# Kernel tuning notes

Measured on AMD Instinct MI355X. Metric: run time of the kernel, lower is better.

## Reference

```python
import jax, jax.numpy as jnp
import numpy as np

B, S, E, H = 4, 2048, 512, 8
DK = E // H
LN_EPS = 1e-5


def setup_inputs() -> dict:
    key = jax.random.key(0)
    ks = jax.random.split(key, 12)
    s_in = 1.0 / np.sqrt(E)
    inp = {
        "Q": jax.random.normal(ks[0], (B, S, E), jnp.float32),
        "K": jax.random.normal(ks[1], (B, S, E), jnp.float32),
        "V": jax.random.normal(ks[2], (B, S, E), jnp.float32),
        # per-head projection weights stacked over heads: [H, E, DK]
        "Wq": jax.random.normal(ks[3], (H, E, DK), jnp.float32) * s_in,
        "bq": jnp.zeros((H, DK), jnp.float32),
        "Wk": jax.random.normal(ks[4], (H, E, DK), jnp.float32) * s_in,
        "bk": jnp.zeros((H, DK), jnp.float32),
        "Wv": jax.random.normal(ks[5], (H, E, DK), jnp.float32) * s_in,
        "bv": jnp.zeros((H, DK), jnp.float32),
        # final linear: [E, E]
        "Wf": jax.random.normal(ks[6], (E, E), jnp.float32) * s_in,
        "bf": jnp.zeros((E,), jnp.float32),
        "gamma": jnp.ones((E,), jnp.float32),
        "beta": jnp.zeros((E,), jnp.float32),
    }
    return inp


def reference(Q, K, V, Wq, bq, Wk, bk, Wv, bv, Wf, bf, gamma, beta):
    scale = DK ** (-0.5)
    # batched per-head projections: [B,H,S,DK]
    q = jnp.einsum("bse,hed->bhsd", Q, Wq) + bq[None, :, None, :]
    k = jnp.einsum("bse,hed->bhsd", K, Wk) + bk[None, :, None, :]
    v = jnp.einsum("bse,hed->bhsd", V, Wv) + bv[None, :, None, :]
    # full QK^T scores [B,H,S,S], scaled, softmax over key axis (dim=2 of bmm == last)
    scores = jnp.einsum("bhsd,bhtd->bhst", q, k) * scale
    attn = jax.nn.softmax(scores, axis=-1)
    ctx = jnp.einsum("bhst,bhtd->bhsd", attn, v)
    # concat heads along feature dim -> [B,S,E]
    z = jnp.transpose(ctx, (0, 2, 1, 3)).reshape(B, S, E)
    residual = jnp.einsum("bse,ef->bsf", z, Wf) + bf
    x = Q + residual
    mean = jnp.mean(x, axis=-1, keepdims=True)
    var = jnp.mean(jnp.square(x - mean), axis=-1, keepdims=True)
    out = (x - mean) * jax.lax.rsqrt(var + LN_EPS) * gamma + beta
    return out
```

## Files before the change

### kernel.cpp

```cpp
#include <hip/hip_runtime.h>
#include <hip/hip_bf16.h>

#define Bb 4
#define Ss 2048
#define Ee 512
#define Hh 8
#define DKk 64

typedef __bf16 bf16_t;
typedef bf16_t bf16x8 __attribute__((ext_vector_type(8)));
typedef bf16_t bf16x4 __attribute__((ext_vector_type(4)));
typedef float f32x4 __attribute__((ext_vector_type(4)));
typedef float f32x16 __attribute__((ext_vector_type(16)));

#define MFMA16(a, b, c) __builtin_amdgcn_mfma_f32_16x16x32_bf16(a, b, c, 0, 0, 0)
#define MFMA32(a, b, c) __builtin_amdgcn_mfma_f32_32x32x16_bf16(a, b, c, 0, 0, 0)

#define GLOAD16(src, dst)                                          \
  __builtin_amdgcn_global_load_lds(                                \
      (const __attribute__((address_space(1))) void*)(src),        \
      (__attribute__((address_space(3))) void*)(dst), 16, 0, 0)

#define LO4(v) __builtin_shufflevector(v, v, 0, 1, 2, 3)
#define HI4(v) __builtin_shufflevector(v, v, 4, 5, 6, 7)

static __device__ __forceinline__ bf16_t f2bf(float f) { return (bf16_t)f; }

static __device__ __forceinline__ float fast_exp2(float x) {
#if __has_builtin(__builtin_amdgcn_exp2f)
  return __builtin_amdgcn_exp2f(x);
#else
  return exp2f(x);
#endif
}

static __device__ __forceinline__ unsigned cvtpk(float lo, float hi) {
  unsigned r;
  asm("v_cvt_pk_bf16_f32 %0, %1, %2" : "=v"(r) : "v"(lo), "v"(hi));
  return r;
}
static __device__ __forceinline__ void plswap(unsigned& a, unsigned& b) {
  asm("v_permlane32_swap_b32 %0, %1" : "+v"(a), "+v"(b));
}

__global__ __launch_bounds__(256) void cvt_k(const float* __restrict__ Q,
                                             const float* __restrict__ K,
                                             const float* __restrict__ V,
                                             bf16_t* __restrict__ dst) {
  int which = blockIdx.x >> 11;
  int bi = blockIdx.x & 2047;
  const float* src = (which == 0) ? Q : ((which == 1) ? K : V);
  bf16_t* d = dst + (size_t)which * ((size_t)Bb * Ss * Ee);
  size_t idx = ((size_t)bi * 256 + threadIdx.x) * 8;
  float4 a = *(const float4*)(src + idx);
  float4 b = *(const float4*)(src + idx + 4);
  bf16x8 o;
  o[0] = f2bf(a.x); o[1] = f2bf(a.y); o[2] = f2bf(a.z); o[3] = f2bf(a.w);
  o[4] = f2bf(b.x); o[5] = f2bf(b.y); o[6] = f2bf(b.z); o[7] = f2bf(b.w);
  *(bf16x8*)(d + idx) = o;
}

__global__ __launch_bounds__(256) void pack_weights_k(
    const float* __restrict__ Wq, const float* __restrict__ Wk,
    const float* __restrict__ Wv, const float* __restrict__ Wf,
    bf16_t* __restrict__ Wt, bf16_t* __restrict__ Wft) {
  __shared__ float tile[64][65];
  int t = threadIdx.x;
  int y = blockIdx.y;
  const float* sp;
  bf16_t* dp;
  int sR, r0, c0;
  if (y < 24) {
    int mat = y >> 3, h = y & 7;
    const float* W = (mat == 0) ? Wq : ((mat == 1) ? Wk : Wv);
    sp = W + (size_t)h * (Ee * DKk);
    sR = 64;
    dp = Wt + (size_t)mat * (Ee * Ee) + (size_t)(h * 64) * Ee;
    r0 = blockIdx.x * 64;
    c0 = 0;
  } else {
    sp = Wf;
    sR = 512;
    dp = Wft;
    r0 = blockIdx.x * 64;
    c0 = (y - 24) * 64;
  }
  int lr = t >> 2, seg = t & 3;
  const float* sprow = sp + (size_t)(r0 + lr) * sR + c0 + seg * 16;
  float4 f0 = ((const float4*)sprow)[0];
  float4 f1 = ((const float4*)sprow)[1];
  float4 f2 = ((const float4*)sprow)[2];
  float4 f3 = ((const float4*)sprow)[3];
  tile[lr][seg * 16 + 0] = f0.x;  tile[lr][seg * 16 + 1] = f0.y;
  tile[lr][seg * 16 + 2] = f0.z;  tile[lr][seg * 16 + 3] = f0.w;
  tile[lr][seg * 16 + 4] = f1.x;  tile[lr][seg * 16 + 5] = f1.y;
  tile[lr][seg * 16 + 6] = f1.z;  tile[lr][seg * 16 + 7] = f1.w;
  tile[lr][seg * 16 + 8] = f2.x;  tile[lr][seg * 16 + 9] = f2.y;
  tile[lr][seg * 16 + 10] = f2.z; tile[lr][seg * 16 + 11] = f2.w;
  tile[lr][seg * 16 + 12] = f3.x; tile[lr][seg * 16 + 13] = f3.y;
  tile[lr][seg * 16 + 14] = f3.z; tile[lr][seg * 16 + 15] = f3.w;
  __syncthreads();
  bf16x8 o0, o1;
#pragma unroll
  for (int i = 0; i < 8; i++) {
    o0[i] = f2bf(tile[seg * 16 + i][lr]);
    o1[i] = f2bf(tile[seg * 16 + 8 + i][lr]);
  }
  bf16_t* dst = dp + (size_t)(c0 + lr) * Ee + r0 + seg * 16;
  *(bf16x8*)dst = o0;
  *(bf16x8*)(dst + 8) = o1;
}

__global__ __launch_bounds__(256) void vt_k(const bf16_t* __restrict__ vsrc,
                                            bf16_t* __restrict__ vtG) {
  __shared__ bf16_t tile[64][68];
  const int t = threadIdx.x;
  const int bh = blockIdx.y;
  const int s0 = blockIdx.x * 64;
  const bf16_t* vp = vsrc + (size_t)bh * (Ss * DKk);
  const int r = t >> 2, seg = t & 3;
  const bf16_t* src = vp + (size_t)(s0 + r) * DKk + seg * 16;
  bf16x8 a = ((const bf16x8*)src)[0];
  bf16x8 b = ((const bf16x8*)src)[1];
  bf16_t* ld = &tile[r][seg * 16];
  *(bf16x4*)(ld + 0) = LO4(a); *(bf16x4*)(ld + 4) = HI4(a);
  *(bf16x4*)(ld + 8) = LO4(b); *(bf16x4*)(ld + 12) = HI4(b);
  __syncthreads();
  bf16x8 o0, o1;
#pragma unroll
  for (int j = 0; j < 8; j++) {
    o0[j] = tile[seg * 16 + j][r];
    o1[j] = tile[seg * 16 + 8 + j][r];
  }
  bf16_t* dst = vtG + (size_t)bh * ((size_t)DKk * Ss) + (size_t)r * Ss + s0 + seg * 16;
  *(bf16x8*)dst = o0;
  *(bf16x8*)(dst + 8) = o1;
}

__global__ __launch_bounds__(256) void proj_gemm_k(
    const bf16_t* __restrict__ Xb3, const bf16_t* __restrict__ Wt,
    const float* __restrict__ bq, const float* __restrict__ bk,
    const float* __restrict__ bv, bf16_t* __restrict__ qkv) {
  __shared__ bf16_t As[128 * 64];
  __shared__ bf16_t Bs[128 * 64];
  const int t = threadIdx.x;
  const int zb = blockIdx.z;
  const bf16_t* Ap = Wt + (size_t)zb * (Ee * Ee);
  const bf16_t* Bp = Xb3 + (size_t)zb * ((size_t)Bb * Ss * Ee);
  const float* bias = (zb == 0) ? bq : ((zb == 1) ? bk : bv);
  bf16_t* Outp = qkv + (size_t)zb * ((size_t)Bb * Hh * Ss * DKk);
  const float scl = (zb == 0) ? 0.18033688f : 1.0f;
  const int id = blockIdx.x + (blockIdx.y << 2);
  const int nid = (id & 7) * 32 + (id >> 3);
  const int n0 = (nid & 3) * 128;
  const int m0 = (nid >> 2) * 128;
  const int lane = t & 63, w = t >> 6;
  const int wn = w >> 1, wm = w & 1;
  const int rsel = lane & 15, grp = lane >> 4;
  const int wbase = (t & ~63);

  f32x4 acc[4][4];
#pragma unroll
  for (int ni = 0; ni < 4; ni++)
#pragma unroll
    for (int mi = 0; mi < 4; mi++) acc[ni][mi] = (f32x4){0.f, 0.f, 0.f, 0.f};

  for (int k0 = 0; k0 < Ee; k0 += 64) {
#pragma unroll
    for (int i = 0; i < 4; i++) {
      int slot = i * 256 + t;
      int row = slot >> 3;
      int g = (slot & 7) ^ (row & 7);
      GLOAD16(Ap + (size_t)(n0 + row) * Ee + k0 + g * 8,
              As + (size_t)(i * 256 + wbase) * 8);
      GLOAD16(Bp + (size_t)(m0 + row) * Ee + k0 + g * 8,
              Bs + (size_t)(i * 256 + wbase) * 8);
    }
    __syncthreads();
#pragma unroll
    for (int kk = 0; kk < 2; kk++) {
      bf16x8 af[4], bff[4];
#pragma unroll
      for (int ni = 0; ni < 4; ni++) {
        int arow = wn * 64 + ni * 16 + rsel;
        int c = ((kk * 4 + grp) ^ (arow & 7)) * 8;
        af[ni] = *(const bf16x8*)&As[arow * 64 + c];
      }
#pragma unroll
      for (int mi = 0; mi < 4; mi++) {
        int brow = wm * 64 + mi * 16 + rsel;
        int c = ((kk * 4 + grp) ^ (brow & 7)) * 8;
        bff[mi] = *(const bf16x8*)&Bs[brow * 64 + c];
      }
#pragma unroll
      for (int ni = 0; ni < 4; ni++)
#pragma unroll
        for (int mi = 0; mi < 4; mi++)
          acc[ni][mi] = MFMA16(af[ni], bff[mi], acc[ni][mi]);
    }
    __syncthreads();
  }

#pragma unroll
  for (int ni = 0; ni < 4; ni++) {
    int nb = n0 + wn * 64 + ni * 16 + grp * 4;
    float4 b4 = *(const float4*)(bias + nb);
    const float* b4p = (const float*)&b4;
    int hh = nb >> 6, dd = nb & 63;
#pragma unroll
    for (int mi = 0; mi < 4; mi++) {
      int m = m0 + wm * 64 + mi * 16 + rsel;
      int bI = m >> 11, sI = m & 2047;
      bf16x4 o;
#pragma unroll
      for (int r = 0; r < 4; r++)
        o[r] = f2bf((acc[ni][mi][r] + b4p[r]) * scl);
      *(bf16x4*)(Outp + (((size_t)(bI * Hh + hh)) * Ss + sI) * DKk + dd) = o;
    }
  }
}

__global__ __launch_bounds__(256) void final_gemm_k(
    const bf16_t* __restrict__ zin, const bf16_t* __restrict__ Wft,
    const float* __restrict__ bfb, const float* __restrict__ Qres,
    float* __restrict__ x) {
  __shared__ bf16_t As[128 * 64];
  __shared__ bf16_t Bs[128 * 64];
  const int t = threadIdx.x;
  const int id = blockIdx.x + (blockIdx.y << 2);
  const int nid = (id & 7) * 32 + (id >> 3);
  const int n0 = (nid & 3) * 128;
  const int m0 = (nid >> 2) * 128;
  const int lane = t & 63, w = t >> 6;
  const int wn = w >> 1, wm = w & 1;
  const int rsel = lane & 15, grp = lane >> 4;
  const int wbase = (t & ~63);

  f32x4 acc[4][4];
#pragma unroll
  for (int ni = 0; ni < 4; ni++)
#pragma unroll
    for (int mi = 0; mi < 4; mi++) acc[ni][mi] = (f32x4){0.f, 0.f, 0.f, 0.f};

  for (int k0 = 0; k0 < Ee; k0 += 64) {
#pragma unroll
    for (int i = 0; i < 4; i++) {
      int slot = i * 256 + t;
      int row = slot >> 3;
      int g = (slot & 7) ^ (row & 7);
      GLOAD16(Wft + (size_t)(n0 + row) * Ee + k0 + g * 8,
              As + (size_t)(i * 256 + wbase) * 8);
      GLOAD16(zin + (size_t)(m0 + row) * Ee + k0 + g * 8,
              Bs + (size_t)(i * 256 + wbase) * 8);
    }
    __syncthreads();
#pragma unroll
    for (int kk = 0; kk < 2; kk++) {
      bf16x8 af[4], bff[4];
#pragma unroll
      for (int ni = 0; ni < 4; ni++) {
        int arow = wn * 64 + ni * 16 + rsel;
        int c = ((kk * 4 + grp) ^ (arow & 7)) * 8;
        af[ni] = *(const bf16x8*)&As[arow * 64 + c];
      }
#pragma unroll
      for (int mi = 0; mi < 4; mi++) {
        int brow = wm * 64 + mi * 16 + rsel;
        int c = ((kk * 4 + grp) ^ (brow & 7)) * 8;
        bff[mi] = *(const bf16x8*)&Bs[brow * 64 + c];
      }
#pragma unroll
      for (int ni = 0; ni < 4; ni++)
#pragma unroll
        for (int mi = 0; mi < 4; mi++)
          acc[ni][mi] = MFMA16(af[ni], bff[mi], acc[ni][mi]);
    }
    __syncthreads();
  }

#pragma unroll
  for (int ni = 0; ni < 4; ni++) {
    int nb = n0 + wn * 64 + ni * 16 + grp * 4;
    float4 b4 = *(const float4*)(bfb + nb);
#pragma unroll
    for (int mi = 0; mi < 4; mi++) {
      int m = m0 + wm * 64 + mi * 16 + rsel;
      float4 q4 = *(const float4*)(Qres + (size_t)m * Ee + nb);
      float4 o;
      o.x = acc[ni][mi][0] + b4.x + q4.x;
      o.y = acc[ni][mi][1] + b4.y + q4.y;
      o.z = acc[ni][mi][2] + b4.z + q4.z;
      o.w = acc[ni][mi][3] + b4.w + q4.w;
      *(float4*)(x + (size_t)m * Ee + nb) = o;
    }
  }
}

__global__ __launch_bounds__(512, 4) void attn_k(const bf16_t* __restrict__ qkv,
                                                 const bf16_t* __restrict__ vtG,
                                                 bf16_t* __restrict__ zout) {
  const size_t HS = (size_t)Bb * Hh * Ss * DKk;
  __shared__ __align__(16) unsigned char smem_raw[2 * 34816];
  bf16_t (*Ks)[2][64][68] = reinterpret_cast<bf16_t (*)[2][64][68]>(smem_raw);
  bf16_t (*Vt)[2][64][68] = reinterpret_cast<bf16_t (*)[2][64][68]>(smem_raw + 34816);
  const int t = threadIdx.x, w = t >> 6, lane = t & 63;
  const int qsub = w >> 1, half = w & 1;
  const int ql = lane & 31, hi = lane >> 5;
  const int bh = blockIdx.y;
  const bf16_t* qp = qkv + (size_t)bh * (Ss * DKk);
  const bf16_t* kp = qp + HS;
  const bf16_t* vt = vtG + (size_t)bh * ((size_t)DKk * Ss);
  const int qrow = blockIdx.x * 128 + qsub * 32 + ql;

  bf16x8 qf0 = *(const bf16x8*)(qp + (size_t)qrow * DKk + 0 + hi * 8);
  bf16x8 qf1 = *(const bf16x8*)(qp + (size_t)qrow * DKk + 16 + hi * 8);
  bf16x8 qf2 = *(const bf16x8*)(qp + (size_t)qrow * DKk + 32 + hi * 8);
  bf16x8 qf3 = *(const bf16x8*)(qp + (size_t)qrow * DKk + 48 + hi * 8);

  const int sid = qsub * 64 + lane;
  const int srow = sid >> 2, sseg = sid & 3;
  const int koff0 = half * (Ss / 2);

  f32x16 ctx0, ctx1;
#pragma unroll
  for (int r = 0; r < 16; r++) { ctx0[r] = 0.f; ctx1[r] = 0.f; }
  float m_run = -1e30f, l_run = 0.f;

  {
    const bf16_t* ksrc = kp + (size_t)(koff0 + srow) * DKk + sseg * 16;
    bf16x8 ka = ((const bf16x8*)ksrc)[0], kb = ((const bf16x8*)ksrc)[1];
    const bf16_t* vsrc = vt + (size_t)srow * Ss + koff0 + sseg * 16;
    bf16x8 va = ((const bf16x8*)vsrc)[0], vb = ((const bf16x8*)vsrc)[1];
    bf16_t* kd = &Ks[half][0][srow][sseg * 16];
    *(bf16x4*)(kd + 0) = LO4(ka); *(bf16x4*)(kd + 4) = HI4(ka);
    *(bf16x4*)(kd + 8) = LO4(kb); *(bf16x4*)(kd + 12) = HI4(kb);
    bf16_t* vd = &Vt[half][0][srow][sseg * 16];
    *(bf16x4*)(vd + 0) = LO4(va); *(bf16x4*)(vd + 4) = HI4(va);
    *(bf16x4*)(vd + 8) = LO4(vb); *(bf16x4*)(vd + 12) = HI4(vb);
  }
  __syncthreads();

  const int NT = (Ss / 2) / 64;
  bf16x8 pk0, pk1, pv0, pv1;
  for (int it = 0; it < NT; ++it) {
    const int cb = it & 1;
    if (it < NT - 1) {
      const int k0 = koff0 + (it + 1) * 64;
      const bf16_t* ksrc = kp + (size_t)(k0 + srow) * DKk + sseg * 16;
      pk0 = ((const bf16x8*)ksrc)[0]; pk1 = ((const bf16x8*)ksrc)[1];
      const bf16_t* vsrc = vt + (size_t)srow * Ss + k0 + sseg * 16;
      pv0 = ((const bf16x8*)vsrc)[0]; pv1 = ((const bf16x8*)vsrc)[1];
    }

    f32x16 st0, st1;
#pragma unroll
    for (int r = 0; r < 16; r++) { st0[r] = 0.f; st1[r] = 0.f; }
    __builtin_amdgcn_s_setprio(1);
#pragma unroll
    for (int s = 0; s < 4; s++) {
      bf16x4 a0 = *(const bf16x4*)&Ks[half][cb][ql][s * 16 + hi * 8];
      bf16x4 a1 = *(const bf16x4*)&Ks[half][cb][ql][s * 16 + hi * 8 + 4];
      bf16x8 af = __builtin_shufflevector(a0, a1, 0, 1, 2, 3, 4, 5, 6, 7);
      bf16x4 c0 = *(const bf16x4*)&Ks[half][cb][32 + ql][s * 16 + hi * 8];
      bf16x4 c1 = *(const bf16x4*)&Ks[half][cb][32 + ql][s * 16 + hi * 8 + 4];
      bf16x8 af2 = __builtin_shufflevector(c0, c1, 0, 1, 2, 3, 4, 5, 6, 7);
      bf16x8 qf = (s == 0) ? qf0 : ((s == 1) ? qf1 : ((s == 2) ? qf2 : qf3));
      st0 = MFMA32(af, qf, st0);
      st1 = MFMA32(af2, qf, st1);
    }
    __builtin_amdgcn_s_setprio(0);

    float mx = st0[0];
#pragma unroll
    for (int r = 1; r < 16; r++) mx = fmaxf(mx, st0[r]);
#pragma unroll
    for (int r = 0; r < 16; r++) mx = fmaxf(mx, st1[r]);
    mx = fmaxf(mx, __shfl_xor(mx, 32));
    if (__any(mx > m_run + 8.0f)) {
      float mn = fmaxf(m_run, mx);
      float sc = fast_exp2(m_run - mn);
      l_run *= sc;
#pragma unroll
      for (int r = 0; r < 16; r++) { ctx0[r] *= sc; ctx1[r] *= sc; }
      m_run = mn;
    }
    float ps = 0.f;
#pragma unroll
    for (int r = 0; r < 16; r++) { st0[r] = fast_exp2(st0[r] - m_run); ps += st0[r]; }
#pragma unroll
    for (int r = 0; r < 16; r++) { st1[r] = fast_exp2(st1[r] - m_run); ps += st1[r]; }
    ps += __shfl_xor(ps, 32);
    l_run += ps;

    union U { unsigned u[4]; bf16x8 v; };
    U F00, F01, F10, F11;
    {
      unsigned x0 = cvtpk(st0[0], st0[1]), y0 = cvtpk(st0[4], st0[5]); plswap(x0, y0);
      unsigned x1 = cvtpk(st0[2], st0[3]), y1 = cvtpk(st0[6], st0[7]); plswap(x1, y1);
      F00.u[0] = x0; F00.u[1] = x1; F00.u[2] = y0; F00.u[3] = y1;
      unsigned x2 = cvtpk(st0[8], st0[9]), y2 = cvtpk(st0[12], st0[13]); plswap(x2, y2);
      unsigned x3 = cvtpk(st0[10], st0[11]), y3 = cvtpk(st0[14], st0[15]); plswap(x3, y3);
      F01.u[0] = x2; F01.u[1] = x3; F01.u[2] = y2; F01.u[3] = y3;
      unsigned x4 = cvtpk(st1[0], st1[1]), y4 = cvtpk(st1[4], st1[5]); plswap(x4, y4);
      unsigned x5 = cvtpk(st1[2], st1[3]), y5 = cvtpk(st1[6], st1[7]); plswap(x5, y5);
      F10.u[0] = x4; F10.u[1] = x5; F10.u[2] = y4; F10.u[3] = y5;
      unsigned x6 = cvtpk(st1[8], st1[9]), y6 = cvtpk(st1[12], st1[13]); plswap(x6, y6);
      unsigned x7 = cvtpk(st1[10], st1[11]), y7 = cvtpk(st1[14], st1[15]); plswap(x7, y7);
      F11.u[0] = x6; F11.u[1] = x7; F11.u[2] = y6; F11.u[3] = y7;
    }

    auto rdv = [&](int mtrow, int col) -> bf16x8 {
      bf16x4 lo4 = *(const bf16x4*)&Vt[half][cb][mtrow + ql][col + hi * 8];
      bf16x4 hi4 = *(const bf16x4*)&Vt[half][cb][mtrow + ql][col + hi * 8 + 4];
      return __builtin_shufflevector(lo4, hi4, 0, 1, 2, 3, 4, 5, 6, 7);
    };
    __builtin_amdgcn_s_setprio(1);
    ctx0 = MFMA32(rdv(0, 0), F00.v, ctx0);
    ctx0 = MFMA32(rdv(0, 16), F01.v, ctx0);
    ctx0 = MFMA32(rdv(0, 32), F10.v, ctx0);
    ctx0 = MFMA32(rdv(0, 48), F11.v, ctx0);
    ctx1 = MFMA32(rdv(32, 0), F00.v, ctx1);
    ctx1 = MFMA32(rdv(32, 16), F01.v, ctx1);
    ctx1 = MFMA32(rdv(32, 32), F10.v, ctx1);
    ctx1 = MFMA32(rdv(32, 48), F11.v, ctx1);
    __builtin_amdgcn_s_setprio(0);

    if (it < NT - 1) {
      bf16_t* kd = &Ks[half][cb ^ 1][srow][sseg * 16];
      *(bf16x4*)(kd + 0) = LO4(pk0); *(bf16x4*)(kd + 4) = HI4(pk0);
      *(bf16x4*)(kd + 8) = LO4(pk1); *(bf16x4*)(kd + 12) = HI4(pk1);
      bf16_t* vd = &Vt[half][cb ^ 1][srow][sseg * 16];
      *(bf16x4*)(vd + 0) = LO4(pv0); *(bf16x4*)(vd + 4) = HI4(pv0);
      *(bf16x4*)(vd + 8) = LO4(pv1); *(bf16x4*)(vd + 12) = HI4(pv1);
    }
    __syncthreads();
  }

  float* mr = (float*)smem_raw;
  const int msl = qsub * 64 + lane;
  float* cslot = mr + msl * 33;
  float* mym = mr + 8448;
  float* myl = mr + 8704;
  if (half == 1) {
#pragma unroll
    for (int r = 0; r < 16; r++) { cslot[r] = ctx0[r]; cslot[16 + r] = ctx1[r]; }
    mym[msl] = m_run;
    myl[msl] = l_run;
  }
  __syncthreads();
  if (half == 0) {
    float m1 = mym[msl], l1 = myl[msl];
    float mt = fmaxf(m_run, m1);
    float f0 = fast_exp2(m_run - mt), f1 = fast_exp2(m1 - mt);
    float inv = 1.f / (l_run * f0 + l1 * f1);
    const int bI = bh >> 3, hh = bh & 7;
    bf16_t* zr = zout + ((size_t)bI * Ss + qrow) * Ee + hh * 64;
#pragma unroll
    for (int a = 0; a < 4; a++) {
      bf16x4 o0, o1;
#pragma unroll
      for (int b2 = 0; b2 < 4; b2++) {
        o0[b2] = f2bf((ctx0[a * 4 + b2] * f0 + cslot[a * 4 + b2] * f1) * inv);
        o1[b2] = f2bf((ctx1[a * 4 + b2] * f0 + cslot[16 + a * 4 + b2] * f1) * inv);
      }
      *(bf16x4*)(zr + a * 8 + hi * 4) = o0;
      *(bf16x4*)(zr + 32 + a * 8 + hi * 4) = o1;
    }
  }
}

__global__ __launch_bounds__(256) void ln_k(
    const float* __restrict__ x, const float* __restrict__ gamma,
    const float* __restrict__ beta, float* __restrict__ out) {
  int row = blockIdx.x * 4 + (threadIdx.x >> 6);
  int lane = threadIdx.x & 63;
  const float* xr = x + (size_t)row * Ee;
  float4 v0 = *(const float4*)(xr + lane * 8);
  float4 v1 = *(const float4*)(xr + lane * 8 + 4);
  float s = v0.x + v0.y + v0.z + v0.w + v1.x + v1.y + v1.z + v1.w;
  float ss = v0.x * v0.x + v0.y * v0.y + v0.z * v0.z + v0.w * v0.w +
             v1.x * v1.x + v1.y * v1.y + v1.z * v1.z + v1.w * v1.w;
#pragma unroll
  for (int off = 32; off >= 1; off >>= 1) {
    s += __shfl_xor(s, off);
    ss += __shfl_xor(ss, off);
  }
  float mean = s * (1.f / 512.f);
  float var = ss * (1.f / 512.f) - mean * mean;
  float inv = rsqrtf(var + 1e-5f);
  float4 g0 = *(const float4*)(gamma + lane * 8);
  float4 g1 = *(const float4*)(gamma + lane * 8 + 4);
  float4 b0 = *(const float4*)(beta + lane * 8);
  float4 b1 = *(const float4*)(beta + lane * 8 + 4);
  float4 o0, o1;
  o0.x = (v0.x - mean) * inv * g0.x + b0.x;
  o0.y = (v0.y - mean) * inv * g0.y + b0.y;
  o0.z = (v0.z - mean) * inv * g0.z + b0.z;
  o0.w = (v0.w - mean) * inv * g0.w + b0.w;
  o1.x = (v1.x - mean) * inv * g1.x + b1.x;
  o1.y = (v1.y - mean) * inv * g1.y + b1.y;
  o1.z = (v1.z - mean) * inv * g1.z + b1.z;
  o1.w = (v1.w - mean) * inv * g1.w + b1.w;
  float* orow = out + (size_t)row * Ee;
  *(float4*)(orow + lane * 8) = o0;
  *(float4*)(orow + lane * 8 + 4) = o1;
}

extern "C" void kernel_launch(void* const* d_in, const int* in_sizes, int n_in,
                              void* d_out, int out_size, void* d_ws, size_t ws_size,
                              hipStream_t stream) {
  const float* Q = (const float*)d_in[0];
  const float* K = (const float*)d_in[1];
  const float* V = (const float*)d_in[2];
  const float* Wq = (const float*)d_in[3];
  const float* bq = (const float*)d_in[4];
  const float* Wk = (const float*)d_in[5];
  const float* bk = (const float*)d_in[6];
  const float* Wv = (const float*)d_in[7];
  const float* bv = (const float*)d_in[8];
  const float* Wf = (const float*)d_in[9];
  const float* bfb = (const float*)d_in[10];
  const float* gamma = (const float*)d_in[11];
  const float* beta = (const float*)d_in[12];
  float* out = (float*)d_out;

  bf16_t* Wt = (bf16_t*)d_ws;
  bf16_t* Wft = Wt + 3 * Ee * Ee;
  bf16_t* qkv = Wft + Ee * Ee;
  bf16_t* sA = qkv + (size_t)3 * Bb * Hh * Ss * DKk;
  bf16_t* z = sA;
  bf16_t* vtG = sA + (size_t)Bb * Hh * Ss * DKk;
  float* x = (float*)qkv;

  cvt_k<<<dim3(6144), dim3(256), 0, stream>>>(Q, K, V, sA);
  pack_weights_k<<<dim3(8, 32), dim3(256), 0, stream>>>(Wq, Wk, Wv, Wf, Wt, Wft);
  proj_gemm_k<<<dim3(4, 64, 3), dim3(256), 0, stream>>>(sA, Wt, bq, bk, bv, qkv);
  vt_k<<<dim3(32, 32), dim3(256), 0, stream>>>(qkv + (size_t)2 * Bb * Hh * Ss * DKk, vtG);
  attn_k<<<dim3(16, 32), dim3(512), 0, stream>>>(qkv, vtG, z);
  final_gemm_k<<<dim3(4, 64), dim3(256), 0, stream>>>(z, Wft, bfb, Q, x);
  ln_k<<<dim3(2048), dim3(256), 0, stream>>>(x, gamma, beta, out);
}
```

Before: 208.0 us.

## Fuse input conversion and V transpose into projection GEMM, shrink GEMM tiles

Removes the separate fp32-to-bf16 conversion kernel by having the projection GEMM load fp32 Q/K/V and convert them in registers before writing to LDS. It also removes the V transpose kernel by writing V directly in transposed layout from the GEMM epilogue. GEMM tiles shrink from 128x128 to 64x64 to get more blocks. The intermediate before layer norm is stored as bf16 instead of fp32, and the softmax max/sum reductions are reassociated. The risks are scattered strided stores for V, lower data reuse per tile, and reduced precision in the residual before layer norm.

```diff
diff --git a/kernel.cpp b/kernel.cpp
--- a/kernel.cpp
+++ b/kernel.cpp
@@ -34,6 +34,10 @@
 #endif
 }
 
+static __device__ __forceinline__ float max3f(float a, float b, float c) {
+  return fmaxf(fmaxf(a, b), c);
+}
+
 static __device__ __forceinline__ unsigned cvtpk(float lo, float hi) {
   unsigned r;
   asm("v_cvt_pk_bf16_f32 %0, %1, %2" : "=v"(r) : "v"(lo), "v"(hi));
@@ -41,23 +45,6 @@
 }
 static __device__ __forceinline__ void plswap(unsigned& a, unsigned& b) {
   asm("v_permlane32_swap_b32 %0, %1" : "+v"(a), "+v"(b));
-}
-
-__global__ __launch_bounds__(256) void cvt_k(const float* __restrict__ Q,
-                                             const float* __restrict__ K,
-                                             const float* __restrict__ V,
-                                             bf16_t* __restrict__ dst) {
-  int which = blockIdx.x >> 11;
-  int bi = blockIdx.x & 2047;
-  const float* src = (which == 0) ? Q : ((which == 1) ? K : V);
-  bf16_t* d = dst + (size_t)which * ((size_t)Bb * Ss * Ee);
-  size_t idx = ((size_t)bi * 256 + threadIdx.x) * 8;
-  float4 a = *(const float4*)(src + idx);
-  float4 b = *(const float4*)(src + idx + 4);
-  bf16x8 o;
-  o[0] = f2bf(a.x); o[1] = f2bf(a.y); o[2] = f2bf(a.z); o[3] = f2bf(a.w);
-  o[4] = f2bf(b.x); o[5] = f2bf(b.y); o[6] = f2bf(b.z); o[7] = f2bf(b.w);
-  *(bf16x8*)(d + idx) = o;
 }
 
 __global__ __launch_bounds__(256) void pack_weights_k(
@@ -111,111 +98,117 @@
   *(bf16x8*)(dst + 8) = o1;
 }
 
-__global__ __launch_bounds__(256) void vt_k(const bf16_t* __restrict__ vsrc,
-                                            bf16_t* __restrict__ vtG) {
-  __shared__ bf16_t tile[64][68];
-  const int t = threadIdx.x;
-  const int bh = blockIdx.y;
-  const int s0 = blockIdx.x * 64;
-  const bf16_t* vp = vsrc + (size_t)bh * (Ss * DKk);
-  const int r = t >> 2, seg = t & 3;
-  const bf16_t* src = vp + (size_t)(s0 + r) * DKk + seg * 16;
-  bf16x8 a = ((const bf16x8*)src)[0];
-  bf16x8 b = ((const bf16x8*)src)[1];
-  bf16_t* ld = &tile[r][seg * 16];
-  *(bf16x4*)(ld + 0) = LO4(a); *(bf16x4*)(ld + 4) = HI4(a);
-  *(bf16x4*)(ld + 8) = LO4(b); *(bf16x4*)(ld + 12) = HI4(b);
-  __syncthreads();
-  bf16x8 o0, o1;
-#pragma unroll
-  for (int j = 0; j < 8; j++) {
-    o0[j] = tile[seg * 16 + j][r];
-    o1[j] = tile[seg * 16 + 8 + j][r];
-  }
-  bf16_t* dst = vtG + (size_t)bh * ((size_t)DKk * Ss) + (size_t)r * Ss + s0 + seg * 16;
-  *(bf16x8*)dst = o0;
-  *(bf16x8*)(dst + 8) = o1;
-}
-
 __global__ __launch_bounds__(256) void proj_gemm_k(
-    const bf16_t* __restrict__ Xb3, const bf16_t* __restrict__ Wt,
+    const float* __restrict__ Qi, const float* __restrict__ Ki,
+    const float* __restrict__ Vi, const bf16_t* __restrict__ Wt,
     const float* __restrict__ bq, const float* __restrict__ bk,
-    const float* __restrict__ bv, bf16_t* __restrict__ qkv) {
-  __shared__ bf16_t As[128 * 64];
-  __shared__ bf16_t Bs[128 * 64];
+    const float* __restrict__ bv, bf16_t* __restrict__ qk,
+    bf16_t* __restrict__ vtG) {
+  __shared__ bf16_t As[64 * 64];
+  __shared__ bf16_t Bs[64 * 64];
   const int t = threadIdx.x;
   const int zb = blockIdx.z;
   const bf16_t* Ap = Wt + (size_t)zb * (Ee * Ee);
-  const bf16_t* Bp = Xb3 + (size_t)zb * ((size_t)Bb * Ss * Ee);
+  const float* Bp = (zb == 0) ? Qi : ((zb == 1) ? Ki : Vi);
   const float* bias = (zb == 0) ? bq : ((zb == 1) ? bk : bv);
-  bf16_t* Outp = qkv + (size_t)zb * ((size_t)Bb * Hh * Ss * DKk);
   const float scl = (zb == 0) ? 0.18033688f : 1.0f;
-  const int id = blockIdx.x + (blockIdx.y << 2);
-  const int nid = (id & 7) * 32 + (id >> 3);
-  const int n0 = (nid & 3) * 128;
-  const int m0 = (nid >> 2) * 128;
+  const int id = blockIdx.x + (blockIdx.y << 3);
+  const int nid = (id & 7) * 128 + (id >> 3);
+  const int n0 = (nid & 7) * 64;
+  const int m0 = (nid >> 3) * 64;
   const int lane = t & 63, w = t >> 6;
   const int wn = w >> 1, wm = w & 1;
   const int rsel = lane & 15, grp = lane >> 4;
   const int wbase = (t & ~63);
 
-  f32x4 acc[4][4];
-#pragma unroll
-  for (int ni = 0; ni < 4; ni++)
-#pragma unroll
-    for (int mi = 0; mi < 4; mi++) acc[ni][mi] = (f32x4){0.f, 0.f, 0.f, 0.f};
-
+  f32x4 acc[2][2];
+#pragma unroll
+  for (int ni = 0; ni < 2; ni++)
+#pragma unroll
+    for (int mi = 0; mi < 2; mi++) acc[ni][mi] = (f32x4){0.f, 0.f, 0.f, 0.f};
+
+  const int row2 = t >> 3, j2 = t & 7;
   for (int k0 = 0; k0 < Ee; k0 += 64) {
 #pragma unroll
-    for (int i = 0; i < 4; i++) {
+    for (int i = 0; i < 2; i++) {
       int slot = i * 256 + t;
       int row = slot >> 3;
       int g = (slot & 7) ^ (row & 7);
       GLOAD16(Ap + (size_t)(n0 + row) * Ee + k0 + g * 8,
               As + (size_t)(i * 256 + wbase) * 8);
-      GLOAD16(Bp + (size_t)(m0 + row) * Ee + k0 + g * 8,
-              Bs + (size_t)(i * 256 + wbase) * 8);
+    }
+#pragma unroll
+    for (int i = 0; i < 2; i++) {
+      int row = row2 + i * 32;
+      int g = j2 ^ (row & 7);
+      const float* src = Bp + (size_t)(m0 + row) * Ee + k0 + g * 8;
+      float4 fa = ((const float4*)src)[0];
+      float4 fb = ((const float4*)src)[1];
+      union { unsigned u[4]; bf16x8 v; } P;
+      P.u[0] = cvtpk(fa.x, fa.y); P.u[1] = cvtpk(fa.z, fa.w);
+      P.u[2] = cvtpk(fb.x, fb.y); P.u[3] = cvtpk(fb.z, fb.w);
+      *(bf16x8*)&Bs[(row * 8 + j2) * 8] = P.v;
     }
     __syncthreads();
 #pragma unroll
     for (int kk = 0; kk < 2; kk++) {
-      bf16x8 af[4], bff[4];
-#pragma unroll
-      for (int ni = 0; ni < 4; ni++) {
-        int arow = wn * 64 + ni * 16 + rsel;
+      bf16x8 af[2], bff[2];
+#pragma unroll
+      for (int ni = 0; ni < 2; ni++) {
+        int arow = wn * 32 + ni * 16 + rsel;
         int c = ((kk * 4 + grp) ^ (arow & 7)) * 8;
         af[ni] = *(const bf16x8*)&As[arow * 64 + c];
       }
 #pragma unroll
-      for (int mi = 0; mi < 4; mi++) {
-        int brow = wm * 64 + mi * 16 + rsel;
+      for (int mi = 0; mi < 2; mi++) {
+        int brow = wm * 32 + mi * 16 + rsel;
         int c = ((kk * 4 + grp) ^ (brow & 7)) * 8;
         bff[mi] = *(const bf16x8*)&Bs[brow * 64 + c];
       }
 #pragma unroll
-      for (int ni = 0; ni < 4; ni++)
-#pragma unroll
-        for (int mi = 0; mi < 4; mi++)
+      for (int ni = 0; ni < 2; ni++)
+#pragma unroll
+        for (int mi = 0; mi < 2; mi++)
           acc[ni][mi] = MFMA16(af[ni], bff[mi], acc[ni][mi]);
     }
     __syncthreads();
   }
 
-#pragma unroll
-  for (int ni = 0; ni < 4; ni++) {
-    int nb = n0 + wn * 64 + ni * 16 + grp * 4;
-    float4 b4 = *(const float4*)(bias + nb);
-    const float* b4p = (const float*)&b4;
-    int hh = nb >> 6, dd = nb & 63;
-#pragma unroll
-    for (int mi = 0; mi < 4; mi++) {
-      int m = m0 + wm * 64 + mi * 16 + rsel;
-      int bI = m >> 11, sI = m & 2047;
-      bf16x4 o;
-#pragma unroll
-      for (int r = 0; r < 4; r++)
-        o[r] = f2bf((acc[ni][mi][r] + b4p[r]) * scl);
-      *(bf16x4*)(Outp + (((size_t)(bI * Hh + hh)) * Ss + sI) * DKk + dd) = o;
+  if (zb < 2) {
+    bf16_t* Outp = qk + (size_t)zb * ((size_t)Bb * Hh * Ss * DKk);
+#pragma unroll
+    for (int ni = 0; ni < 2; ni++) {
+      int nb = n0 + wn * 32 + ni * 16 + grp * 4;
+      float4 b4 = *(const float4*)(bias + nb);
+      const float* b4p = (const float*)&b4;
+      int hh = nb >> 6, dd = nb & 63;
+#pragma unroll
+      for (int mi = 0; mi < 2; mi++) {
+        int m = m0 + wm * 32 + mi * 16 + rsel;
+        int bI = m >> 11, sI = m & 2047;
+        bf16x4 o;
+#pragma unroll
+        for (int r = 0; r < 4; r++)
+          o[r] = f2bf((acc[ni][mi][r] + b4p[r]) * scl);
+        *(bf16x4*)(Outp + (((size_t)(bI * Hh + hh)) * Ss + sI) * DKk + dd) = o;
+      }
+    }
+  } else {
+#pragma unroll
+    for (int ni = 0; ni < 2; ni++) {
+      int nb = n0 + wn * 32 + ni * 16 + grp * 4;
+      float4 b4 = *(const float4*)(bias + nb);
+      const float* b4p = (const float*)&b4;
+      int hh = nb >> 6, dd = nb & 63;
+#pragma unroll
+      for (int mi = 0; mi < 2; mi++) {
+        int m = m0 + wm * 32 + mi * 16 + rsel;
+        int bI = m >> 11, sI = m & 2047;
+        bf16_t* base = vtG + (((size_t)(bI * Hh + hh)) * 64 + dd) * Ss + sI;
+#pragma unroll
+        for (int r = 0; r < 4; r++)
+          base[(size_t)r * Ss] = f2bf(acc[ni][mi][r] + b4p[r]);
+      }
     }
   }
 }
@@ -223,28 +216,28 @@
 __global__ __launch_bounds__(256) void final_gemm_k(
     const bf16_t* __restrict__ zin, const bf16_t* __restrict__ Wft,
     const float* __restrict__ bfb, const float* __restrict__ Qres,
-    float* __restrict__ x) {
-  __shared__ bf16_t As[128 * 64];
-  __shared__ bf16_t Bs[128 * 64];
+    bf16_t* __restrict__ x) {
+  __shared__ bf16_t As[64 * 64];
+  __shared__ bf16_t Bs[64 * 64];
   const int t = threadIdx.x;
-  const int id = blockIdx.x + (blockIdx.y << 2);
-  const int nid = (id & 7) * 32 + (id >> 3);
-  const int n0 = (nid & 3) * 128;
-  const int m0 = (nid >> 2) * 128;
+  const int id = blockIdx.x + (blockIdx.y << 3);
+  const int nid = (id & 7) * 128 + (id >> 3);
+  const int n0 = (nid & 7) * 64;
+  const int m0 = (nid >> 3) * 64;
   const int lane = t & 63, w = t >> 6;
   const int wn = w >> 1, wm = w & 1;
   const int rsel = lane & 15, grp = lane >> 4;
   const int wbase = (t & ~63);
 
-  f32x4 acc[4][4];
-#pragma unroll
-  for (int ni = 0; ni < 4; ni++)
-#pragma unroll
-    for (int mi = 0; mi < 4; mi++) acc[ni][mi] = (f32x4){0.f, 0.f, 0.f, 0.f};
+  f32x4 acc[2][2];
+#pragma unroll
+  for (int ni = 0; ni < 2; ni++)
+#pragma unroll
+    for (int mi = 0; mi < 2; mi++) acc[ni][mi] = (f32x4){0.f, 0.f, 0.f, 0.f};
 
   for (int k0 = 0; k0 < Ee; k0 += 64) {
 #pragma unroll
-    for (int i = 0; i < 4; i++) {
+    for (int i = 0; i < 2; i++) {
       int slot = i * 256 + t;
       int row = slot >> 3;
       int g = (slot & 7) ^ (row & 7);
@@ -256,47 +249,47 @@
     __syncthreads();
 #pragma unroll
     for (int kk = 0; kk < 2; kk++) {
-      bf16x8 af[4], bff[4];
-#pragma unroll
-      for (int ni = 0; ni < 4; ni++) {
-        int arow = wn * 64 + ni * 16 + rsel;
+      bf16x8 af[2], bff[2];
+#pragma unroll
+      for (int ni = 0; ni < 2; ni++) {
+        int arow = wn * 32 + ni * 16 + rsel;
         int c = ((kk * 4 + grp) ^ (arow & 7)) * 8;
         af[ni] = *(const bf16x8*)&As[arow * 64 + c];
       }
 #pragma unroll
-      for (int mi = 0; mi < 4; mi++) {
-        int brow = wm * 64 + mi * 16 + rsel;
+      for (int mi = 0; mi < 2; mi++) {
+        int brow = wm * 32 + mi * 16 + rsel;
         int c = ((kk * 4 + grp) ^ (brow & 7)) * 8;
         bff[mi] = *(const bf16x8*)&Bs[brow * 64 + c];
       }
 #pragma unroll
-      for (int ni = 0; ni < 4; ni++)
-#pragma unroll
-        for (int mi = 0; mi < 4; mi++)
+      for (int ni = 0; ni < 2; ni++)
+#pragma unroll
+        for (int mi = 0; mi < 2; mi++)
           acc[ni][mi] = MFMA16(af[ni], bff[mi], acc[ni][mi]);
     }
     __syncthreads();
   }
 
 #pragma unroll
-  for (int ni = 0; ni < 4; ni++) {
-    int nb = n0 + wn * 64 + ni * 16 + grp * 4;
+  for (int ni = 0; ni < 2; ni++) {
+    int nb = n0 + wn * 32 + ni * 16 + grp * 4;
     float4 b4 = *(const float4*)(bfb + nb);
 #pragma unroll
-    for (int mi = 0; mi < 4; mi++) {
-      int m = m0 + wm * 64 + mi * 16 + rsel;
+    for (int mi = 0; mi < 2; mi++) {
+      int m = m0 + wm * 32 + mi * 16 + rsel;
       float4 q4 = *(const float4*)(Qres + (size_t)m * Ee + nb);
-      float4 o;
-      o.x = acc[ni][mi][0] + b4.x + q4.x;
-      o.y = acc[ni][mi][1] + b4.y + q4.y;
-      o.z = acc[ni][mi][2] + b4.z + q4.z;
-      o.w = acc[ni][mi][3] + b4.w + q4.w;
-      *(float4*)(x + (size_t)m * Ee + nb) = o;
-    }
-  }
-}
-
-__global__ __launch_bounds__(512, 4) void attn_k(const bf16_t* __restrict__ qkv,
+      bf16x4 o;
+      o[0] = f2bf(acc[ni][mi][0] + b4.x + q4.x);
+      o[1] = f2bf(acc[ni][mi][1] + b4.y + q4.y);
+      o[2] = f2bf(acc[ni][mi][2] + b4.z + q4.z);
+      o[3] = f2bf(acc[ni][mi][3] + b4.w + q4.w);
+      *(bf16x4*)(x + (size_t)m * Ee + nb) = o;
+    }
+  }
+}
+
+__global__ __launch_bounds__(512, 4) void attn_k(const bf16_t* __restrict__ qk,
                                                  const bf16_t* __restrict__ vtG,
                                                  bf16_t* __restrict__ zout) {
   const size_t HS = (size_t)Bb * Hh * Ss * DKk;
@@ -307,7 +300,7 @@
   const int qsub = w >> 1, half = w & 1;
   const int ql = lane & 31, hi = lane >> 5;
   const int bh = blockIdx.y;
-  const bf16_t* qp = qkv + (size_t)bh * (Ss * DKk);
+  const bf16_t* qp = qk + (size_t)bh * (Ss * DKk);
   const bf16_t* kp = qp + HS;
   const bf16_t* vt = vtG + (size_t)bh * ((size_t)DKk * Ss);
   const int qrow = blockIdx.x * 128 + qsub * 32 + ql;
@@ -370,11 +363,15 @@
     }
     __builtin_amdgcn_s_setprio(0);
 
-    float mx = st0[0];
-#pragma unroll
-    for (int r = 1; r < 16; r++) mx = fmaxf(mx, st0[r]);
-#pragma unroll
-    for (int r = 0; r < 16; r++) mx = fmaxf(mx, st1[r]);
+    float h[16];
+#pragma unroll
+    for (int r = 0; r < 16; r++) h[r] = fmaxf(st0[r], st1[r]);
+    float p0 = max3f(h[0], h[1], h[2]);
+    float p1 = max3f(h[3], h[4], h[5]);
+    float p2 = max3f(h[6], h[7], h[8]);
+    float p3 = max3f(h[9], h[10], h[11]);
+    float p4 = max3f(h[12], h[13], h[14]);
+    float mx = fmaxf(max3f(p0, p1, p2), max3f(p3, p4, h[15]));
     mx = fmaxf(mx, __shfl_xor(mx, 32));
     if (__any(mx > m_run + 8.0f)) {
       float mn = fmaxf(m_run, mx);
@@ -384,11 +381,12 @@
       for (int r = 0; r < 16; r++) { ctx0[r] *= sc; ctx1[r] *= sc; }
       m_run = mn;
     }
-    float ps = 0.f;
-#pragma unroll
-    for (int r = 0; r < 16; r++) { st0[r] = fast_exp2(st0[r] - m_run); ps += st0[r]; }
-#pragma unroll
-    for (int r = 0; r < 16; r++) { st1[r] = fast_exp2(st1[r] - m_run); ps += st1[r]; }
+    float psA = 0.f, psB = 0.f;
+#pragma unroll
+    for (int r = 0; r < 16; r++) { st0[r] = fast_exp2(st0[r] - m_run); psA += st0[r]; }
+#pragma unroll
+    for (int r = 0; r < 16; r++) { st1[r] = fast_exp2(st1[r] - m_run); psB += st1[r]; }
+    float ps = psA + psB;
     ps += __shfl_xor(ps, 32);
     l_run += ps;
 
@@ -470,16 +468,18 @@
 }
 
 __global__ __launch_bounds__(256) void ln_k(
-    const float* __restrict__ x, const float* __restrict__ gamma,
+    const bf16_t* __restrict__ x, const float* __restrict__ gamma,
     const float* __restrict__ beta, float* __restrict__ out) {
   int row = blockIdx.x * 4 + (threadIdx.x >> 6);
   int lane = threadIdx.x & 63;
-  const float* xr = x + (size_t)row * Ee;
-  float4 v0 = *(const float4*)(xr + lane * 8);
-  float4 v1 = *(const float4*)(xr + lane * 8 + 4);
-  float s = v0.x + v0.y + v0.z + v0.w + v1.x + v1.y + v1.z + v1.w;
-  float ss = v0.x * v0.x + v0.y * v0.y + v0.z * v0.z + v0.w * v0.w +
-             v1.x * v1.x + v1.y * v1.y + v1.z * v1.z + v1.w * v1.w;
+  const bf16_t* xr = x + (size_t)row * Ee + lane * 8;
+  bf16x8 xv = *(const bf16x8*)xr;
+  float v[8];
+#pragma unroll
+  for (int i = 0; i < 8; i++) v[i] = (float)xv[i];
+  float s = 0.f, ss = 0.f;
+#pragma unroll
+  for (int i = 0; i < 8; i++) { s += v[i]; ss += v[i] * v[i]; }
 #pragma unroll
   for (int off = 32; off >= 1; off >>= 1) {
     s += __shfl_xor(s, off);
@@ -493,14 +493,14 @@
   float4 b0 = *(const float4*)(beta + lane * 8);
   float4 b1 = *(const float4*)(beta + lane * 8 + 4);
   float4 o0, o1;
-  o0.x = (v0.x - mean) * inv * g0.x + b0.x;
-  o0.y = (v0.y - mean) * inv * g0.y + b0.y;
-  o0.z = (v0.z - mean) * inv * g0.z + b0.z;
-  o0.w = (v0.w - mean) * inv * g0.w + b0.w;
-  o1.x = (v1.x - mean) * inv * g1.x + b1.x;
-  o1.y = (v1.y - mean) * inv * g1.y + b1.y;
-  o1.z = (v1.z - mean) * inv * g1.z + b1.z;
-  o1.w = (v1.w - mean) * inv * g1.w + b1.w;
+  o0.x = (v[0] - mean) * inv * g0.x + b0.x;
+  o0.y = (v[1] - mean) * inv * g0.y + b0.y;
+  o0.z = (v[2] - mean) * inv * g0.z + b0.z;
+  o0.w = (v[3] - mean) * inv * g0.w + b0.w;
+  o1.x = (v[4] - mean) * inv * g1.x + b1.x;
+  o1.y = (v[5] - mean) * inv * g1.y + b1.y;
+  o1.z = (v[6] - mean) * inv * g1.z + b1.z;
+  o1.w = (v[7] - mean) * inv * g1.w + b1.w;
   float* orow = out + (size_t)row * Ee;
   *(float4*)(orow + lane * 8) = o0;
   *(float4*)(orow + lane * 8 + 4) = o1;
@@ -526,17 +526,15 @@
 
   bf16_t* Wt = (bf16_t*)d_ws;
   bf16_t* Wft = Wt + 3 * Ee * Ee;
-  bf16_t* qkv = Wft + Ee * Ee;
-  bf16_t* sA = qkv + (size_t)3 * Bb * Hh * Ss * DKk;
-  bf16_t* z = sA;
-  bf16_t* vtG = sA + (size_t)Bb * Hh * Ss * DKk;
-  float* x = (float*)qkv;
-
-  cvt_k<<<dim3(6144), dim3(256), 0, stream>>>(Q, K, V, sA);
+  bf16_t* qk = Wft + Ee * Ee;
+  bf16_t* vtG = qk + (size_t)2 * Bb * Hh * Ss * DKk;
+  bf16_t* z = vtG + (size_t)Bb * Hh * Ss * DKk;
+  bf16_t* x = z + (size_t)Bb * Ss * Ee;
+
   pack_weights_k<<<dim3(8, 32), dim3(256), 0, stream>>>(Wq, Wk, Wv, Wf, Wt, Wft);
-  proj_gemm_k<<<dim3(4, 64, 3), dim3(256), 0, stream>>>(sA, Wt, bq, bk, bv, qkv);
-  vt_k<<<dim3(32, 32), dim3(256), 0, stream>>>(qkv + (size_t)2 * Bb * Hh * Ss * DKk, vtG);
-  attn_k<<<dim3(16, 32), dim3(512), 0, stream>>>(qkv, vtG, z);
-  final_gemm_k<<<dim3(4, 64), dim3(256), 0, stream>>>(z, Wft, bfb, Q, x);
+  proj_gemm_k<<<dim3(8, 128, 3), dim3(256), 0, stream>>>(Q, K, V, Wt, bq, bk, bv,
+                                                         qk, vtG);
+  attn_k<<<dim3(16, 32), dim3(512), 0, stream>>>(qk, vtG, z);
+  final_gemm_k<<<dim3(8, 128), dim3(256), 0, stream>>>(z, Wft, bfb, Q, x);
   ln_k<<<dim3(2048), dim3(256), 0, stream>>>(x, gamma, beta, out);
 }
```

Result: slower. 215.6 us (+3.7%).
